# Performance work log

Hardware: AMD Instinct MI355X
Metric: run time of the kernel (lower is better)

## Reference

```python
import jax, jax.numpy as jnp
import numpy as np

H = 51  # hidden size fixed by the module

def _gru_cell(x, h, w_ih, w_hh, b_ih, b_hh):
    # PyTorch GRUCell math. w_ih: [3H, in], w_hh: [3H, H]
    gi = x @ w_ih.T + b_ih          # [B, 3H]
    gh = h @ w_hh.T + b_hh          # [B, 3H]
    i_r, i_z, i_n = jnp.split(gi, 3, axis=-1)
    h_r, h_z, h_n = jnp.split(gh, 3, axis=-1)
    r = jax.nn.sigmoid(i_r + h_r)
    z = jax.nn.sigmoid(i_z + h_z)
    n = jnp.tanh(i_n + r * h_n)
    return (1.0 - z) * n + z * h


def setup_inputs() -> dict:
    key = jax.random.key(0)
    ks = jax.random.split(key, 11)
    B, T = 2048, 1000
    s = 1.0 / np.sqrt(H)  # torch default init scale
    u = lambda k, shape: jax.random.uniform(k, shape, jnp.float32, -s, s)
    return {
        "x": jax.random.normal(ks[0], (B, T), jnp.float32),
        "w_ih1": u(ks[1], (3 * H, 1)),
        "w_hh1": u(ks[2], (3 * H, H)),
        "b_ih1": u(ks[3], (3 * H,)),
        "b_hh1": u(ks[4], (3 * H,)),
        "w_ih2": u(ks[5], (3 * H, H)),
        "w_hh2": u(ks[6], (3 * H, H)),
        "b_ih2": u(ks[7], (3 * H,)),
        "b_hh2": u(ks[8], (3 * H,)),
        "w_lin": u(ks[9], (1, H)),
        "b_lin": u(ks[10], (1,)),
        "future_steps": 1000,
    }


def reference(x, w_ih1, w_hh1, b_ih1, b_hh1, w_ih2, w_hh2, b_ih2, b_hh2,
              w_lin, b_lin, future_steps):
    B = x.shape[0]
    h1 = jnp.zeros((B, H), x.dtype)
    h2 = jnp.zeros((B, H), x.dtype)

    def step(carry, xt):  # xt: [B, 1]
        h1, h2 = carry
        h1 = _gru_cell(xt, h1, w_ih1, w_hh1, b_ih1, b_hh1)
        h2 = _gru_cell(h1, h2, w_ih2, w_hh2, b_ih2, b_hh2)
        out = h2 @ w_lin.T + b_lin  # [B, 1]
        return (h1, h2), out

    xs = jnp.swapaxes(x, 0, 1)[:, :, None]  # [T, B, 1]
    (h1, h2), outs1 = jax.lax.scan(step, (h1, h2), xs)

    def fstep(carry, _):
        h1, h2, out = carry
        h1 = _gru_cell(out, h1, w_ih1, w_hh1, b_ih1, b_hh1)
        h2 = _gru_cell(h1, h2, w_ih2, w_hh2, b_ih2, b_hh2)
        out = h2 @ w_lin.T + b_lin
        return (h1, h2, out), out

    last = outs1[-1]
    (_, _, _), outs2 = jax.lax.scan(fstep, (h1, h2, last), None,
                                    length=future_steps)

    outs = jnp.concatenate([outs1, outs2], axis=0)  # [T+F, B, 1]
    return jnp.swapaxes(outs[:, :, 0], 0, 1)        # [B, T+F]
```

## Files before the change

### kernel.cpp

```cpp
#include <hip/hip_runtime.h>
#include <hip/hip_bf16.h>

#define HH 51
#define TPB 512
#define BPB 8
#define US 36

typedef _Float16 half8 __attribute__((ext_vector_type(8)));
typedef float f4 __attribute__((ext_vector_type(4)));

#define LBAR() asm volatile("s_waitcnt lgkmcnt(0)\ns_barrier" ::: "memory")

__device__ __forceinline__ float bf2f(unsigned short u) {
    return __uint_as_float(((unsigned)u) << 16);
}
__device__ __forceinline__ float loadf(const void* p, size_t i, bool bf) {
    return bf ? bf2f(((const unsigned short*)p)[i]) : ((const float*)p)[i];
}
__device__ __forceinline__ void storef(void* p, size_t i, float v, bool bf) {
    if (bf) ((__hip_bfloat16*)p)[i] = __float2bfloat16(v);
    else    ((float*)p)[i] = v;
}
__device__ __forceinline__ float sigm(float v) {
    return __builtin_amdgcn_rcpf(1.0f + __expf(-v));
}
__device__ __forceinline__ float tanh_fast(float v) {
    return fmaf(2.0f, __builtin_amdgcn_rcpf(1.0f + __expf(-2.0f * v)), -1.0f);
}
__device__ __forceinline__ f4 MF(half8 a, half8 b, f4 c) {
    return __builtin_amdgcn_mfma_f32_16x16x32_f16(a, b, c, 0, 0, 0);
}
__device__ __forceinline__ float wave_sum(float x) {
    float s = x, t;
    t = __builtin_bit_cast(float, __builtin_amdgcn_update_dpp(0, __builtin_bit_cast(int, s), 0x111, 0xf, 0xf, true)); s += t;
    t = __builtin_bit_cast(float, __builtin_amdgcn_update_dpp(0, __builtin_bit_cast(int, s), 0x112, 0xf, 0xf, true)); s += t;
    t = __builtin_bit_cast(float, __builtin_amdgcn_update_dpp(0, __builtin_bit_cast(int, s), 0x114, 0xf, 0xf, true)); s += t;
    t = __builtin_bit_cast(float, __builtin_amdgcn_update_dpp(0, __builtin_bit_cast(int, s), 0x118, 0xf, 0xf, true)); s += t;
    t = __builtin_bit_cast(float, __builtin_amdgcn_update_dpp(0, __builtin_bit_cast(int, s), 0x142, 0xa, 0xf, true)); s += t;
    t = __builtin_bit_cast(float, __builtin_amdgcn_update_dpp(0, __builtin_bit_cast(int, s), 0x143, 0xc, 0xf, true)); s += t;
    return __builtin_bit_cast(float, __builtin_amdgcn_readlane(__builtin_bit_cast(int, s), 63));
}
__device__ __forceinline__ float rdlane(float v, int idx) {
    return __builtin_bit_cast(float, __builtin_amdgcn_readlane(__builtin_bit_cast(int, v), idx));
}

__global__ __launch_bounds__(TPB, 1) void gru_kernel(
    const void* __restrict__ xg,
    const void* __restrict__ wih1, const void* __restrict__ whh1,
    const void* __restrict__ bih1, const void* __restrict__ bhh1,
    const void* __restrict__ wih2, const void* __restrict__ whh2,
    const void* __restrict__ bih2, const void* __restrict__ bhh2,
    const void* __restrict__ wlin, const void* __restrict__ blin_p,
    void* __restrict__ dout, int T, int TF)
{
    __shared__ __align__(16) _Float16 stg[208 * 64];
    __shared__ __align__(16) float gbuf1[52 * US];
    __shared__ __align__(16) float gbuf2[52 * US];
    __shared__ __align__(16) _Float16 h1b[16 * 72];
    __shared__ __align__(16) _Float16 h2b[16 * 72];
    __shared__ float obufL[BPB * 36];

    const int tid = threadIdx.x, w = tid >> 6, lane = tid & 63;
    const int n16 = lane & 15, q = lane >> 4;
    const bool li = lane < HH;
    const int il = li ? lane : HH - 1;
    const int bg0 = blockIdx.x * BPB;
    const int myb = bg0 + w;

    bool isbf;
    {
        const unsigned short* u = (const unsigned short*)whh1;
        int ok = 1;
#pragma unroll
        for (int k = 0; k < 16; ++k) {
            unsigned e = (u[2 * k] >> 7) & 0xFF;
            ok &= (e >= 100 && e <= 125) ? 1 : 0;
        }
        isbf = (ok != 0);
    }

    float wr1 = 0, wz1 = 0, wn1 = 0, wl = 0;
    if (li) {
        wr1 = loadf(wih1, il, isbf);          wz1 = loadf(wih1, HH + il, isbf);
        wn1 = loadf(wih1, 2 * HH + il, isbf); wl = loadf(wlin, il, isbf);
    }
    const float blv = loadf(blin_p, 0, isbf);

    const int nM1 = (w < 3) ? 3 : (w < 5) ? 2 : 0;
    const int bM1 = (w < 3) ? w * 3 : 9 + (w - 3) * 2;
    const int nM2 = (w < 4) ? 1 : (w < 7) ? 2 : 3;
    const int bM2 = (w < 4) ? w : (w < 7) ? 4 + (w - 4) * 2 : 10;
    const int laneoff = q * US + 4 * n16;
    const bool stlane = (n16 < 8);

    half8 WfM1[3][2], WfM2[3][4];

#pragma unroll 1
    for (int ps = 0; ps < 3; ++ps) {
        for (int e = tid; e < 208 * 64; e += TPB) {
            int r = e >> 6, k = e & 63;
            int u = r >> 2, g = r & 3;
            float v = 0.0f;
            if (ps == 0) {
                if (u < HH) {
                    if (g < 2) {
                        int gr = g * HH + u;
                        if (k < HH) v = loadf(whh1, (size_t)gr * HH + k, isbf);
                        else if (k == 52) v = loadf(bhh1, gr, isbf) + loadf(bih1, gr, isbf);
                        else if (k == 53) v = loadf(wih1, gr, isbf);
                    } else if (g == 2) {
                        int gr = 2 * HH + u;
                        if (k < HH) v = loadf(whh1, (size_t)gr * HH + k, isbf);
                        else if (k == 52) v = loadf(bhh1, gr, isbf);
                    } else {
                        int gr = 2 * HH + u;
                        if (k == 52) v = loadf(bih1, gr, isbf);
                        else if (k == 53) v = loadf(wih1, gr, isbf);
                    }
                }
            } else if (ps == 1) {
                if (u < HH) {
                    if (g < 2) {
                        int gr = g * HH + u;
                        if (k < HH) v = loadf(whh2, (size_t)gr * HH + k, isbf);
                        else if (k == 52) v = loadf(bhh2, gr, isbf) + loadf(bih2, gr, isbf);
                    } else if (g == 2) {
                        int gr = 2 * HH + u;
                        if (k < HH) v = loadf(whh2, (size_t)gr * HH + k, isbf);
                        else if (k == 52) v = loadf(bhh2, gr, isbf);
                    } else {
                        if (k == 52) v = loadf(bih2, 2 * HH + u, isbf);
                    }
                } else if (r == 204) {
                    if (k < HH) v = loadf(wlin, k, isbf);
                    else if (k == 52) v = blv;
                }
            } else {
                if (u < HH) {
                    if (g < 2) {
                        if (k < HH) v = loadf(wih2, (size_t)(g * HH + u) * HH + k, isbf);
                    } else if (g == 3) {
                        if (k < HH) v = loadf(wih2, (size_t)(2 * HH + u) * HH + k, isbf);
                    }
                }
            }
            stg[e] = (_Float16)v;
        }
        __syncthreads();
        if (ps == 0) {
#pragma unroll
            for (int s = 0; s < 3; ++s) if (s < nM1) {
                int tl = bM1 + s;
                WfM1[s][0] = *(const half8*)(stg + (size_t)(16 * tl + n16) * 64 + q * 8);
                WfM1[s][1] = *(const half8*)(stg + (size_t)(16 * tl + n16) * 64 + 32 + q * 8);
            }
        } else if (ps == 1) {
#pragma unroll
            for (int s = 0; s < 3; ++s) if (s < nM2) {
                int tl = bM2 + s;
                WfM2[s][0] = *(const half8*)(stg + (size_t)(16 * tl + n16) * 64 + q * 8);
                WfM2[s][1] = *(const half8*)(stg + (size_t)(16 * tl + n16) * 64 + 32 + q * 8);
            }
        } else {
#pragma unroll
            for (int s = 0; s < 3; ++s) if (s < nM2) {
                int tl = bM2 + s;
                WfM2[s][2] = *(const half8*)(stg + (size_t)(16 * tl + n16) * 64 + q * 8);
                WfM2[s][3] = *(const half8*)(stg + (size_t)(16 * tl + n16) * 64 + 32 + q * 8);
            }
        }
        __syncthreads();
    }

    for (int e = tid; e < 16 * 72; e += TPB) { h1b[e] = (_Float16)0; h2b[e] = (_Float16)0; }
    for (int e = tid; e < 52 * US; e += TPB) { gbuf1[e] = 0.0f; gbuf2[e] = 0.0f; }

    float xreg = 0.0f, xnext = 0.0f;
    if (lane < T) xreg = loadf(xg, (size_t)myb * T + lane, isbf);
    __syncthreads();
    if (tid < 16) { h1b[tid * 72 + 52] = (_Float16)1.0f; h2b[tid * 72 + 52] = (_Float16)1.0f; }
    if (lane == 0) h1b[w * 72 + 53] = (_Float16)rdlane(xreg, 0);
    __syncthreads();

    {
        half8 H10 = *(const half8*)(h1b + n16 * 72 + q * 8);
        half8 H11 = *(const half8*)(h1b + n16 * 72 + 32 + q * 8);
#pragma unroll
        for (int s = 0; s < 3; ++s) if (s < nM1) {
            f4 a = {0.f, 0.f, 0.f, 0.f};
            a = MF(WfM1[s][0], H10, a); a = MF(WfM1[s][1], H11, a);
            if (stlane) *(f4*)(gbuf1 + (bM1 + s) * 4 * US + laneoff) = a;
        }
    }
    __syncthreads();

    float h1p = 0.0f, h2p = 0.0f;
    const float* gl1 = gbuf1 + il * US + 4 * w;
    const float* gl2 = gbuf2 + il * US + 4 * w;
    const int or2 = 51 * US;

    for (int t = 0; t < T; ++t) {
        f4 G1 = *(const f4*)gl1;
        {
            int ni = (t + 1) & 63;
            float xsrc = (ni == 0) ? xnext : xreg;
            float xnv = (t == T - 1) ? 0.0f : rdlane(xsrc, ni);
            if (lane == 0) h1b[w * 72 + 53] = (_Float16)xnv;
        }
        {
            float r = sigm(G1[0]);
            float z = sigm(G1[1]);
            float n = tanh_fast(fmaf(r, G1[2], G1[3]));
            float h = fmaf(z, h1p - n, n); h1p = h;
            if (li) h1b[w * 72 + il] = (_Float16)h;
        }
        if (t > 0) {
            f4 G2 = *(const f4*)gl2;
            float r2 = sigm(G2[0]), z2 = sigm(G2[1]);
            float n2 = tanh_fast(fmaf(r2, G2[2], G2[3]));
            float h = fmaf(z2, h2p - n2, n2); h2p = h;
            if (li) h2b[w * 72 + il] = (_Float16)h;
        }
        if (lane == 0 && t >= 2)
            obufL[w * 36 + ((t - 2) & 31)] = gbuf2[or2 + 4 * w];
        LBAR();

        {
            half8 H10 = *(const half8*)(h1b + n16 * 72 + q * 8);
            half8 H11 = *(const half8*)(h1b + n16 * 72 + 32 + q * 8);
            half8 H20 = *(const half8*)(h2b + n16 * 72 + q * 8);
            half8 H21 = *(const half8*)(h2b + n16 * 72 + 32 + q * 8);
#pragma unroll
            for (int s = 0; s < 3; ++s) if (s < nM1) {
                f4 a = {0.f, 0.f, 0.f, 0.f};
                a = MF(WfM1[s][0], H10, a); a = MF(WfM1[s][1], H11, a);
                if (stlane) *(f4*)(gbuf1 + (bM1 + s) * 4 * US + laneoff) = a;
            }
#pragma unroll
            for (int s = 0; s < 3; ++s) if (s < nM2) {
                f4 a = {0.f, 0.f, 0.f, 0.f}, b = {0.f, 0.f, 0.f, 0.f};
                a = MF(WfM2[s][0], H20, a); a = MF(WfM2[s][1], H21, a);
                b = MF(WfM2[s][2], H10, b); b = MF(WfM2[s][3], H11, b);
                a = a + b;
                if (stlane) *(f4*)(gbuf2 + (bM2 + s) * 4 * US + laneoff) = a;
            }
        }
        if (w >= 6 && (t & 31) == 1 && t > 32) {
            int fb = t - 33;
#pragma unroll
            for (int k2 = 0; k2 < 2; ++k2) {
                int et = ((w - 6) << 7) + (k2 << 6) + lane;
                int b = et >> 5, tt = et & 31;
                storef(dout, (size_t)(bg0 + b) * TF + fb + tt, obufL[b * 36 + tt], isbf);
            }
        }
        if ((t & 63) == 0) {
            int base = t + 64;
            if (base < T) {
                int src = base + lane;
                xnext = (src < T) ? loadf(xg, (size_t)myb * T + src, isbf) : 0.0f;
            }
        } else if ((t & 63) == 63) {
            xreg = xnext;
        }
        LBAR();
    }

    for (int t = T; t < TF; ++t) {
        f4 G1 = *(const f4*)gl1;
        f4 G2 = *(const f4*)gl2;
        if (t == T && lane == 0)
            obufL[w * 36 + ((t - 2) & 31)] = gbuf2[or2 + 4 * w];
        {
            float r2 = sigm(G2[0]), z2 = sigm(G2[1]);
            float n2 = tanh_fast(fmaf(r2, G2[2], G2[3]));
            float h = fmaf(z2, h2p - n2, n2); h2p = h;
            float p = 0.0f;
            if (li) {
                h2b[w * 72 + il] = (_Float16)h;
                p = h * wl;
            }
            float outv = wave_sum(p) + blv;
            if (lane == 0) obufL[w * 36 + ((t - 1) & 31)] = outv;
            float r = sigm(fmaf(outv, wr1, G1[0]));
            float z = sigm(fmaf(outv, wz1, G1[1]));
            float n = tanh_fast(fmaf(r, G1[2], fmaf(outv, wn1, G1[3])));
            float h1 = fmaf(z, h1p - n, n); h1p = h1;
            if (li) h1b[w * 72 + il] = (_Float16)h1;
        }
        LBAR();
        {
            half8 H10 = *(const half8*)(h1b + n16 * 72 + q * 8);
            half8 H11 = *(const half8*)(h1b + n16 * 72 + 32 + q * 8);
            half8 H20 = *(const half8*)(h2b + n16 * 72 + q * 8);
            half8 H21 = *(const half8*)(h2b + n16 * 72 + 32 + q * 8);
#pragma unroll
            for (int s = 0; s < 3; ++s) if (s < nM1) {
                f4 a = {0.f, 0.f, 0.f, 0.f};
                a = MF(WfM1[s][0], H10, a); a = MF(WfM1[s][1], H11, a);
                if (stlane) *(f4*)(gbuf1 + (bM1 + s) * 4 * US + laneoff) = a;
            }
#pragma unroll
            for (int s = 0; s < 3; ++s) if (s < nM2) {
                f4 a = {0.f, 0.f, 0.f, 0.f}, b = {0.f, 0.f, 0.f, 0.f};
                a = MF(WfM2[s][0], H20, a); a = MF(WfM2[s][1], H21, a);
                b = MF(WfM2[s][2], H10, b); b = MF(WfM2[s][3], H11, b);
                a = a + b;
                if (stlane) *(f4*)(gbuf2 + (bM2 + s) * 4 * US + laneoff) = a;
            }
        }
        if (w >= 6 && (t & 31) == 0) {
            int fb = t - 32;
#pragma unroll
            for (int k2 = 0; k2 < 2; ++k2) {
                int et = ((w - 6) << 7) + (k2 << 6) + lane;
                int b = et >> 5, tt = et & 31;
                storef(dout, (size_t)(bg0 + b) * TF + fb + tt, obufL[b * 36 + tt], isbf);
            }
        }
        LBAR();
    }

    {
        f4 G2 = *(const f4*)gl2;
        float p = 0.0f;
        float r2 = sigm(G2[0]), z2 = sigm(G2[1]);
        float n2 = tanh_fast(fmaf(r2, G2[2], G2[3]));
        float h = fmaf(z2, h2p - n2, n2);
        if (li) p = h * wl;
        float osum = wave_sum(p) + blv;
        if (lane == 0) obufL[w * 36 + ((TF - 1) & 31)] = osum;
    }
    __syncthreads();
    {
        int base = (TF - 1) & ~31, rem = TF - base;
        if (tid < BPB * 32) {
            int b = tid >> 5, tt = tid & 31;
            if (tt < rem)
                storef(dout, (size_t)(bg0 + b) * TF + base + tt, obufL[b * 36 + tt], isbf);
        }
    }
}

extern "C" void kernel_launch(void* const* d_in, const int* in_sizes, int n_in,
                              void* d_out, int out_size, void* d_ws, size_t ws_size,
                              hipStream_t stream) {
    const int B = 2048;
    const int T = in_sizes[0] / B;
    const int TF = out_size / B;
    gru_kernel<<<dim3(B / BPB), dim3(TPB), 0, stream>>>(
        d_in[0], d_in[1], d_in[2], d_in[3], d_in[4], d_in[5],
        d_in[6], d_in[7], d_in[8], d_in[9], d_in[10],
        d_out, T, TF);
}
```

Baseline: 1.783 ms.

## Fuse gate nonlinearity into MFMA owner waves with double-buffered hidden state

In the teacher-forced phase, each wave now applies the GRU gate nonlinearities directly on its MFMA accumulator tiles, so gate pre-activations no longer go through a shared gbuf. Hidden states are double-buffered in LDS, which cuts the per-step barriers from two to one. The MFMA tile assignment is rebalanced to at most two tiles per layer per wave, and the output buffer grows to 64 entries. The cost is uneven work across waves, plus a handoff block that rebuilds gbuf and the per-lane hidden state before the autoregressive phase.

```diff
diff --git a/kernel.cpp b/kernel.cpp
--- a/kernel.cpp
+++ b/kernel.cpp
@@ -56,9 +56,10 @@
     __shared__ __align__(16) _Float16 stg[208 * 64];
     __shared__ __align__(16) float gbuf1[52 * US];
     __shared__ __align__(16) float gbuf2[52 * US];
-    __shared__ __align__(16) _Float16 h1b[16 * 72];
-    __shared__ __align__(16) _Float16 h2b[16 * 72];
-    __shared__ float obufL[BPB * 36];
+    __shared__ __align__(16) _Float16 h1T[2][16 * 72];
+    __shared__ __align__(16) _Float16 h2T[2][16 * 72];
+    __shared__ float obufL[BPB * 64];
+    __shared__ float hfin[2][BPB * 52];
 
     const int tid = threadIdx.x, w = tid >> 6, lane = tid & 63;
     const int n16 = lane & 15, q = lane >> 4;
@@ -86,14 +87,18 @@
     }
     const float blv = loadf(blin_p, 0, isbf);
 
-    const int nM1 = (w < 3) ? 3 : (w < 5) ? 2 : 0;
-    const int bM1 = (w < 3) ? w * 3 : 9 + (w - 3) * 2;
-    const int nM2 = (w < 4) ? 1 : (w < 7) ? 2 : 3;
-    const int bM2 = (w < 4) ? w : (w < 7) ? 4 + (w - 4) * 2 : 10;
+    const int nm1 = (w < 5) ? 2 : 1;
+    int m2a, m2b, nm2;
+    if (w < 2)      { m2a = w + 3; m2b = w + 11; nm2 = 2; }
+    else if (w < 5) { m2a = w + 3; m2b = 0;      nm2 = 1; }
+    else            { m2a = w - 5; m2b = w + 3;  nm2 = 2; }
+    const int m1t[2] = { w, w + 8 };
+    const int m2t[2] = { m2a, m2b };
     const int laneoff = q * US + 4 * n16;
     const bool stlane = (n16 < 8);
-
-    half8 WfM1[3][2], WfM2[3][4];
+    const bool outw = (w == 1);
+
+    half8 WfM1[2][2], WfM2[2][4];
 
 #pragma unroll 1
     for (int ps = 0; ps < 3; ++ps) {
@@ -149,109 +154,93 @@
         __syncthreads();
         if (ps == 0) {
 #pragma unroll
-            for (int s = 0; s < 3; ++s) if (s < nM1) {
-                int tl = bM1 + s;
-                WfM1[s][0] = *(const half8*)(stg + (size_t)(16 * tl + n16) * 64 + q * 8);
-                WfM1[s][1] = *(const half8*)(stg + (size_t)(16 * tl + n16) * 64 + 32 + q * 8);
+            for (int i = 0; i < 2; ++i) if (i < nm1) {
+                int tl = m1t[i];
+                WfM1[i][0] = *(const half8*)(stg + (size_t)(16 * tl + n16) * 64 + q * 8);
+                WfM1[i][1] = *(const half8*)(stg + (size_t)(16 * tl + n16) * 64 + 32 + q * 8);
             }
         } else if (ps == 1) {
 #pragma unroll
-            for (int s = 0; s < 3; ++s) if (s < nM2) {
-                int tl = bM2 + s;
-                WfM2[s][0] = *(const half8*)(stg + (size_t)(16 * tl + n16) * 64 + q * 8);
-                WfM2[s][1] = *(const half8*)(stg + (size_t)(16 * tl + n16) * 64 + 32 + q * 8);
+            for (int i = 0; i < 2; ++i) if (i < nm2) {
+                int tl = m2t[i];
+                WfM2[i][0] = *(const half8*)(stg + (size_t)(16 * tl + n16) * 64 + q * 8);
+                WfM2[i][1] = *(const half8*)(stg + (size_t)(16 * tl + n16) * 64 + 32 + q * 8);
             }
         } else {
 #pragma unroll
-            for (int s = 0; s < 3; ++s) if (s < nM2) {
-                int tl = bM2 + s;
-                WfM2[s][2] = *(const half8*)(stg + (size_t)(16 * tl + n16) * 64 + q * 8);
-                WfM2[s][3] = *(const half8*)(stg + (size_t)(16 * tl + n16) * 64 + 32 + q * 8);
+            for (int i = 0; i < 2; ++i) if (i < nm2) {
+                int tl = m2t[i];
+                WfM2[i][2] = *(const half8*)(stg + (size_t)(16 * tl + n16) * 64 + q * 8);
+                WfM2[i][3] = *(const half8*)(stg + (size_t)(16 * tl + n16) * 64 + 32 + q * 8);
             }
         }
         __syncthreads();
     }
 
-    for (int e = tid; e < 16 * 72; e += TPB) { h1b[e] = (_Float16)0; h2b[e] = (_Float16)0; }
-    for (int e = tid; e < 52 * US; e += TPB) { gbuf1[e] = 0.0f; gbuf2[e] = 0.0f; }
-
+    for (int e = tid; e < 16 * 72; e += TPB) {
+        h1T[0][e] = (_Float16)0; h1T[1][e] = (_Float16)0;
+        h2T[0][e] = (_Float16)0; h2T[1][e] = (_Float16)0;
+    }
     float xreg = 0.0f, xnext = 0.0f;
     if (lane < T) xreg = loadf(xg, (size_t)myb * T + lane, isbf);
     __syncthreads();
-    if (tid < 16) { h1b[tid * 72 + 52] = (_Float16)1.0f; h2b[tid * 72 + 52] = (_Float16)1.0f; }
-    if (lane == 0) h1b[w * 72 + 53] = (_Float16)rdlane(xreg, 0);
+    if (tid < 16) {
+        h1T[0][tid * 72 + 52] = (_Float16)1.0f; h1T[1][tid * 72 + 52] = (_Float16)1.0f;
+        h2T[0][tid * 72 + 52] = (_Float16)1.0f; h2T[1][tid * 72 + 52] = (_Float16)1.0f;
+    }
+    if (lane == 0) h1T[1][w * 72 + 53] = (_Float16)rdlane(xreg, 0);
     __syncthreads();
 
-    {
-        half8 H10 = *(const half8*)(h1b + n16 * 72 + q * 8);
-        half8 H11 = *(const half8*)(h1b + n16 * 72 + 32 + q * 8);
-#pragma unroll
-        for (int s = 0; s < 3; ++s) if (s < nM1) {
-            f4 a = {0.f, 0.f, 0.f, 0.f};
-            a = MF(WfM1[s][0], H10, a); a = MF(WfM1[s][1], H11, a);
-            if (stlane) *(f4*)(gbuf1 + (bM1 + s) * 4 * US + laneoff) = a;
-        }
-    }
-    __syncthreads();
-
-    float h1p = 0.0f, h2p = 0.0f;
-    const float* gl1 = gbuf1 + il * US + 4 * w;
-    const float* gl2 = gbuf2 + il * US + 4 * w;
-    const int or2 = 51 * US;
+    float h1s[2] = {0.f, 0.f}, h2s[2] = {0.f, 0.f};
 
     for (int t = 0; t < T; ++t) {
-        f4 G1 = *(const f4*)gl1;
+        const _Float16* h1r = h1T[(t + 1) & 1];
+        const _Float16* h2r = h2T[(t + 1) & 1];
+        _Float16* h1w = h1T[t & 1];
+        _Float16* h2w = h2T[t & 1];
+        half8 H10 = *(const half8*)(h1r + n16 * 72 + q * 8);
+        half8 H11 = *(const half8*)(h1r + n16 * 72 + 32 + q * 8);
+        half8 H20 = *(const half8*)(h2r + n16 * 72 + q * 8);
+        half8 H21 = *(const half8*)(h2r + n16 * 72 + 32 + q * 8);
         {
             int ni = (t + 1) & 63;
             float xsrc = (ni == 0) ? xnext : xreg;
             float xnv = (t == T - 1) ? 0.0f : rdlane(xsrc, ni);
-            if (lane == 0) h1b[w * 72 + 53] = (_Float16)xnv;
-        }
-        {
-            float r = sigm(G1[0]);
-            float z = sigm(G1[1]);
-            float n = tanh_fast(fmaf(r, G1[2], G1[3]));
-            float h = fmaf(z, h1p - n, n); h1p = h;
-            if (li) h1b[w * 72 + il] = (_Float16)h;
-        }
-        if (t > 0) {
-            f4 G2 = *(const f4*)gl2;
-            float r2 = sigm(G2[0]), z2 = sigm(G2[1]);
-            float n2 = tanh_fast(fmaf(r2, G2[2], G2[3]));
-            float h = fmaf(z2, h2p - n2, n2); h2p = h;
-            if (li) h2b[w * 72 + il] = (_Float16)h;
-        }
-        if (lane == 0 && t >= 2)
-            obufL[w * 36 + ((t - 2) & 31)] = gbuf2[or2 + 4 * w];
-        LBAR();
-
-        {
-            half8 H10 = *(const half8*)(h1b + n16 * 72 + q * 8);
-            half8 H11 = *(const half8*)(h1b + n16 * 72 + 32 + q * 8);
-            half8 H20 = *(const half8*)(h2b + n16 * 72 + q * 8);
-            half8 H21 = *(const half8*)(h2b + n16 * 72 + 32 + q * 8);
-#pragma unroll
-            for (int s = 0; s < 3; ++s) if (s < nM1) {
-                f4 a = {0.f, 0.f, 0.f, 0.f};
-                a = MF(WfM1[s][0], H10, a); a = MF(WfM1[s][1], H11, a);
-                if (stlane) *(f4*)(gbuf1 + (bM1 + s) * 4 * US + laneoff) = a;
-            }
-#pragma unroll
-            for (int s = 0; s < 3; ++s) if (s < nM2) {
-                f4 a = {0.f, 0.f, 0.f, 0.f}, b = {0.f, 0.f, 0.f, 0.f};
-                a = MF(WfM2[s][0], H20, a); a = MF(WfM2[s][1], H21, a);
-                b = MF(WfM2[s][2], H10, b); b = MF(WfM2[s][3], H11, b);
-                a = a + b;
-                if (stlane) *(f4*)(gbuf2 + (bM2 + s) * 4 * US + laneoff) = a;
-            }
-        }
-        if (w >= 6 && (t & 31) == 1 && t > 32) {
-            int fb = t - 33;
+            if (lane == 0) h1w[w * 72 + 53] = (_Float16)xnv;
+        }
+#pragma unroll
+        for (int i = 0; i < 2; ++i) if (i < nm1) {
+            f4 a = {0.f, 0.f, 0.f, 0.f};
+            a = MF(WfM1[i][0], H10, a); a = MF(WfM1[i][1], H11, a);
+            float r = sigm(a[0]), z = sigm(a[1]);
+            float n = tanh_fast(fmaf(r, a[2], a[3]));
+            float h = fmaf(z, h1s[i] - n, n); h1s[i] = h;
+            int u = 4 * m1t[i] + q;
+            if (n16 < 8 && u < HH) h1w[n16 * 72 + u] = (_Float16)h;
+        }
+#pragma unroll
+        for (int i = 0; i < 2; ++i) if (i < nm2) {
+            f4 a = {0.f, 0.f, 0.f, 0.f}, b = {0.f, 0.f, 0.f, 0.f};
+            a = MF(WfM2[i][0], H20, a); a = MF(WfM2[i][1], H21, a);
+            b = MF(WfM2[i][2], H10, b); b = MF(WfM2[i][3], H11, b);
+            a = a + b;
+            if (t > 0) {
+                if (outw && i == 1 && q == 3 && n16 < 8 && t >= 2)
+                    obufL[n16 * 64 + ((t - 2) & 63)] = a[0];
+                float r2 = sigm(a[0]), z2 = sigm(a[1]);
+                float n2 = tanh_fast(fmaf(r2, a[2], a[3]));
+                float h = fmaf(z2, h2s[i] - n2, n2); h2s[i] = h;
+                int u = 4 * m2t[i] + q;
+                if (n16 < 8 && u < HH) h2w[n16 * 72 + u] = (_Float16)h;
+            }
+        }
+        if (w >= 6 && (t & 31) == 2 && t >= 34) {
+            int fb = t - 34;
 #pragma unroll
             for (int k2 = 0; k2 < 2; ++k2) {
                 int et = ((w - 6) << 7) + (k2 << 6) + lane;
-                int b = et >> 5, tt = et & 31;
-                storef(dout, (size_t)(bg0 + b) * TF + fb + tt, obufL[b * 36 + tt], isbf);
+                int b2 = et >> 5, tt = et & 31;
+                storef(dout, (size_t)(bg0 + b2) * TF + fb + tt, obufL[b2 * 64 + ((fb + tt) & 63)], isbf);
             }
         }
         if ((t & 63) == 0) {
@@ -266,47 +255,84 @@
         LBAR();
     }
 
+    const int fbi = (T + 1) & 1;
+    {
+        const _Float16* h1r = h1T[fbi];
+        const _Float16* h2r = h2T[fbi];
+        half8 H10 = *(const half8*)(h1r + n16 * 72 + q * 8);
+        half8 H11 = *(const half8*)(h1r + n16 * 72 + 32 + q * 8);
+        half8 H20 = *(const half8*)(h2r + n16 * 72 + q * 8);
+        half8 H21 = *(const half8*)(h2r + n16 * 72 + 32 + q * 8);
+#pragma unroll
+        for (int i = 0; i < 2; ++i) if (i < nm1) {
+            f4 a = {0.f, 0.f, 0.f, 0.f};
+            a = MF(WfM1[i][0], H10, a); a = MF(WfM1[i][1], H11, a);
+            if (stlane) *(f4*)(gbuf1 + m1t[i] * 4 * US + laneoff) = a;
+            int u = 4 * m1t[i] + q;
+            if (n16 < 8 && u < HH) hfin[0][n16 * 52 + u] = h1s[i];
+        }
+#pragma unroll
+        for (int i = 0; i < 2; ++i) if (i < nm2) {
+            f4 a = {0.f, 0.f, 0.f, 0.f}, b = {0.f, 0.f, 0.f, 0.f};
+            a = MF(WfM2[i][0], H20, a); a = MF(WfM2[i][1], H21, a);
+            b = MF(WfM2[i][2], H10, b); b = MF(WfM2[i][3], H11, b);
+            a = a + b;
+            if (stlane) *(f4*)(gbuf2 + m2t[i] * 4 * US + laneoff) = a;
+            int u = 4 * m2t[i] + q;
+            if (n16 < 8 && u < HH) hfin[1][n16 * 52 + u] = h2s[i];
+        }
+    }
+    __syncthreads();
+
+    float h1p = hfin[0][w * 52 + il];
+    float h2p = hfin[1][w * 52 + il];
+    const float* gl1 = gbuf1 + il * US + 4 * w;
+    const float* gl2 = gbuf2 + il * US + 4 * w;
+    const int or2 = 51 * US;
+    _Float16* fh1 = h1T[fbi];
+    _Float16* fh2 = h2T[fbi];
+
     for (int t = T; t < TF; ++t) {
         f4 G1 = *(const f4*)gl1;
         f4 G2 = *(const f4*)gl2;
         if (t == T && lane == 0)
-            obufL[w * 36 + ((t - 2) & 31)] = gbuf2[or2 + 4 * w];
+            obufL[w * 64 + ((t - 2) & 63)] = gbuf2[or2 + 4 * w];
         {
             float r2 = sigm(G2[0]), z2 = sigm(G2[1]);
             float n2 = tanh_fast(fmaf(r2, G2[2], G2[3]));
             float h = fmaf(z2, h2p - n2, n2); h2p = h;
             float p = 0.0f;
             if (li) {
-                h2b[w * 72 + il] = (_Float16)h;
+                fh2[w * 72 + il] = (_Float16)h;
                 p = h * wl;
             }
             float outv = wave_sum(p) + blv;
-            if (lane == 0) obufL[w * 36 + ((t - 1) & 31)] = outv;
+            if (lane == 0) obufL[w * 64 + ((t - 1) & 63)] = outv;
             float r = sigm(fmaf(outv, wr1, G1[0]));
             float z = sigm(fmaf(outv, wz1, G1[1]));
             float n = tanh_fast(fmaf(r, G1[2], fmaf(outv, wn1, G1[3])));
             float h1 = fmaf(z, h1p - n, n); h1p = h1;
-            if (li) h1b[w * 72 + il] = (_Float16)h1;
+            if (li) fh1[w * 72 + il] = (_Float16)h1;
         }
         LBAR();
         {
-            half8 H10 = *(const half8*)(h1b + n16 * 72 + q * 8);
-            half8 H11 = *(const half8*)(h1b + n16 * 72 + 32 + q * 8);
-            half8 H20 = *(const half8*)(h2b + n16 * 72 + q * 8);
-            half8 H21 = *(const half8*)(h2b + n16 * 72 + 32 + q * 8);
-#pragma unroll
-            for (int s = 0; s < 3; ++s) if (s < nM1) {
+            half8 H10 = *(const half8*)(fh1 + n16 * 72 + q * 8);
+            half8 H11 = *(const half8*)(fh1 + n16 * 72 + 32 + q * 8);
+            half8 H20 = *(const half8*)(fh2 + n16 * 72 + q * 8);
+            half8 H21 = *(const half8*)(fh2 + n16 * 72 + 32 + q * 8);
+#pragma unroll
+            for (int i = 0; i < 2; ++i) if (i < nm1) {
                 f4 a = {0.f, 0.f, 0.f, 0.f};
-                a = MF(WfM1[s][0], H10, a); a = MF(WfM1[s][1], H11, a);
-                if (stlane) *(f4*)(gbuf1 + (bM1 + s) * 4 * US + laneoff) = a;
-            }
-#pragma unroll
-            for (int s = 0; s < 3; ++s) if (s < nM2) {
+                a = MF(WfM1[i][0], H10, a); a = MF(WfM1[i][1], H11, a);
+                if (stlane) *(f4*)(gbuf1 + m1t[i] * 4 * US + laneoff) = a;
+            }
+#pragma unroll
+            for (int i = 0; i < 2; ++i) if (i < nm2) {
                 f4 a = {0.f, 0.f, 0.f, 0.f}, b = {0.f, 0.f, 0.f, 0.f};
-                a = MF(WfM2[s][0], H20, a); a = MF(WfM2[s][1], H21, a);
-                b = MF(WfM2[s][2], H10, b); b = MF(WfM2[s][3], H11, b);
+                a = MF(WfM2[i][0], H20, a); a = MF(WfM2[i][1], H21, a);
+                b = MF(WfM2[i][2], H10, b); b = MF(WfM2[i][3], H11, b);
                 a = a + b;
-                if (stlane) *(f4*)(gbuf2 + (bM2 + s) * 4 * US + laneoff) = a;
+                if (stlane) *(f4*)(gbuf2 + m2t[i] * 4 * US + laneoff) = a;
             }
         }
         if (w >= 6 && (t & 31) == 0) {
@@ -314,8 +340,8 @@
 #pragma unroll
             for (int k2 = 0; k2 < 2; ++k2) {
                 int et = ((w - 6) << 7) + (k2 << 6) + lane;
-                int b = et >> 5, tt = et & 31;
-                storef(dout, (size_t)(bg0 + b) * TF + fb + tt, obufL[b * 36 + tt], isbf);
+                int b2 = et >> 5, tt = et & 31;
+                storef(dout, (size_t)(bg0 + b2) * TF + fb + tt, obufL[b2 * 64 + ((fb + tt) & 63)], isbf);
             }
         }
         LBAR();
@@ -329,15 +355,15 @@
         float h = fmaf(z2, h2p - n2, n2);
         if (li) p = h * wl;
         float osum = wave_sum(p) + blv;
-        if (lane == 0) obufL[w * 36 + ((TF - 1) & 31)] = osum;
+        if (lane == 0) obufL[w * 64 + ((TF - 1) & 63)] = osum;
     }
     __syncthreads();
     {
         int base = (TF - 1) & ~31, rem = TF - base;
         if (tid < BPB * 32) {
-            int b = tid >> 5, tt = tid & 31;
+            int b2 = tid >> 5, tt = tid & 31;
             if (tt < rem)
-                storef(dout, (size_t)(bg0 + b) * TF + base + tt, obufL[b * 36 + tt], isbf);
+                storef(dout, (size_t)(bg0 + b2) * TF + base + tt, obufL[b2 * 64 + ((base + tt) & 63)], isbf);
         }
     }
 }
```

After: 1.609 ms. 1.11x faster.
